# Performance work log

Hardware: AMD Instinct MI355X
Metric: run time of the kernel (lower is better)

The kernel has to match this reference:

```python
import jax, jax.numpy as jnp
import numpy as np

N_WAY = 5
K_SHOT = 5
NBNN_TOPK = 3
TEMPERATURE = 2.0
EPS = 1e-8


def setup_inputs() -> dict:
    key = jax.random.key(0)
    k1, k2, k3 = jax.random.split(key, 3)
    b, q, c, h, w = 4, 75, 640, 11, 11
    s = N_WAY * K_SHOT
    support_xf = jax.random.normal(k1, (b, s, c, h, w), jnp.float32)
    query_xf = jax.random.normal(k2, (b, q, c, h, w), jnp.float32)
    # episodes are ordered class-major: [way0 shots..., way1 shots..., ...]
    support_y = jnp.tile(jnp.repeat(jnp.arange(N_WAY, dtype=jnp.int32), K_SHOT)[None, :], (b, 1))
    query_y = jax.random.randint(k3, (b, q), 0, N_WAY, dtype=jnp.int32)
    return {"support_xf": support_xf, "query_xf": query_xf,
            "support_y": support_y, "query_y": query_y}


def _mn4_loss(support_xf, query_xf, query_y):
    b, s, c, h, w = support_xf.shape
    q = query_xf.shape[1]
    M_q = h * w
    M_s = K_SHOT * h * w

    # ---- InnerproductSimilarity (cosine) ----
    # support: [b, N, c, M_s]  (class-major grouping of shots)
    sf = support_xf.reshape(b, N_WAY, K_SHOT, c, h * w).transpose(0, 1, 3, 2, 4).reshape(b, N_WAY, c, M_s)
    qf = query_xf.reshape(b, q, c, M_q)
    sf = sf / (jnp.linalg.norm(sf, axis=2, keepdims=True) + EPS)
    qf = qf / (jnp.linalg.norm(qf, axis=2, keepdims=True) + EPS)
    # simi: [b, q, N, M_q, M_s]
    simi = jnp.einsum('bqcm,bncs->bqnms', qf, sf)

    # ---- _MNN (compensate_for_single=True branch) ----
    # merged view: [b, q, M_q, N*M_s]
    merged = simi.transpose(0, 1, 3, 2, 4).reshape(b, q, M_q, N_WAY * M_s)
    query_nearest = jnp.argmax(merged, axis=-1)          # [b, q, M_q]
    class_wise_max = simi.max(-1).max(2) + 1.0           # [b, q, M_q]
    class_m = jax.nn.one_hot(query_nearest, N_WAY * M_s, dtype=simi.dtype) * class_wise_max[..., None]
    support_nearest = jnp.argmax(class_m, axis=-2)       # [b, q, N*M_s]
    gathered = jnp.take_along_axis(support_nearest, query_nearest, axis=-1)  # [b, q, M_q]
    q_mask = (gathered == jnp.arange(M_q)[None, None, :])                    # [b, q, M_q]

    # ---- NBNN value: topk over support descriptors, masked sum over query descriptors ----
    topv = jax.lax.top_k(simi, NBNN_TOPK)[0].mean(-1)    # [b, q, N, M_q]
    query_value = (topv * q_mask[:, :, None, :].astype(topv.dtype)).sum(-1)  # [b, q, N]
    logits = query_value.reshape(b * q, N_WAY) / TEMPERATURE

    # ---- cross entropy (mean) ----
    logp = jax.nn.log_softmax(logits, axis=-1)
    y = query_y.reshape(-1)
    loss = -jnp.take_along_axis(logp, y[:, None], axis=1).mean()
    return loss


def reference(support_xf, query_xf, support_y, query_y):
    del support_y  # episodes are class-major by construction
    return _mn4_loss(support_xf, query_xf, query_y)
```

## Files before the change

kernel.cpp:

```cpp
#include <hip/hip_runtime.h>
#include <hip/hip_bf16.h>
#include <math.h>

#define BB 4
#define QQ 75
#define NBQ 300
#define CC 640
#define HW 121
#define NW 5
#define KS 5
#define SS 25
#define MS 605
#define JT 3025
#define NPAIR 38
#define PAIRS_PER_XCD 19

typedef __attribute__((ext_vector_type(8))) short short8;
typedef __attribute__((ext_vector_type(4))) float f32x4;

#define OFF_SBF   0
#define SBF_F     (BB*JT*CC/2)
#define OFF_QBF   (OFF_SBF + SBF_F)
#define QBF_F     (NBQ*HW*CC/2)
#define OFF_P     (OFF_QBF + QBF_F)
#define OFF_NRM   OFF_P

__device__ __forceinline__ void async16(const void* g, void* l) {
    __builtin_amdgcn_global_load_lds(
        (const __attribute__((address_space(1))) unsigned int*)g,
        (__attribute__((address_space(3))) unsigned int*)l, 16, 0, 0);
}

__global__ void norm_kernel(const float* __restrict__ sup, const float* __restrict__ qry,
                            float* __restrict__ nrm, float* __restrict__ out)
{
    const int blk = blockIdx.x;
    const int col = blk >> 2, r = blk & 3;
    const int hw  = threadIdx.x;
    if (blk == 0 && hw == 0) out[0] = 0.f;
    const float* src = (col < BB * SS)
        ? sup + (size_t)col * (CC * HW)
        : qry + (size_t)(col - BB * SS) * (CC * HW);
    float ss = 0.f;
    if (hw < HW) {
        const float* p = src + hw;
#pragma unroll 16
        for (int i = 0; i < CC / 4; ++i) {
            const float v = p[(size_t)(r + i * 4) * HW];
            ss = fmaf(v, v, ss);
        }
    }
    nrm[((size_t)col * 4 + r) * 128 + hw] = ss;
}

__global__ void scale_kernel(const float* __restrict__ sup, const float* __restrict__ qry,
                             const float* __restrict__ nrm,
                             __hip_bfloat16* __restrict__ Sbf, __hip_bfloat16* __restrict__ Qbf)
{
    const int blk = blockIdx.x;
    const int col = blk >> 2, qtr = blk & 3;
    const int t   = threadIdx.x;
    const float* src;
    __hip_bfloat16* dst;
    if (col < BB * SS) {
        const int b = col / SS, s = col % SS;
        const int n = s / KS, k = s % KS;
        src = sup + (size_t)col * (CC * HW);
        dst = Sbf + ((size_t)b * JT + n * MS + k * HW) * CC;
    } else {
        const int bq = col - BB * SS;
        src = qry + (size_t)bq * (CC * HW);
        dst = Qbf + (size_t)bq * (HW * CC);
    }

    __shared__ float inv[128];
    __shared__ float T[32][128];

    if (t < 128) {
        const float p0 = nrm[((size_t)col * 4 + 0) * 128 + t];
        const float p1 = nrm[((size_t)col * 4 + 1) * 128 + t];
        const float p2 = nrm[((size_t)col * 4 + 2) * 128 + t];
        const float p3 = nrm[((size_t)col * 4 + 3) * 128 + t];
        inv[t] = (t < HW) ? 1.f / (sqrtf((p0 + p2) + (p1 + p3)) + 1e-8f) : 0.f;
    }

    for (int it = 0; it < 5; ++it) {
        const int c0 = qtr * 160 + it * 32;
        __syncthreads();
#pragma unroll
        for (int i = 0; i < 16; ++i) {
            int idx = t + i * 256;
            int cc = idx >> 7, hw = idx & 127;
            if (hw < HW) T[cc][hw] = src[(size_t)(c0 + cc) * HW + hw] * inv[hw];
        }
        __syncthreads();
        const int hw = t >> 1, half = t & 1;
        if (hw < HW) {
            __hip_bfloat16 hv[16];
#pragma unroll
            for (int i = 0; i < 16; ++i) hv[i] = __float2bfloat16(T[half * 16 + i][hw]);
            int4* op = reinterpret_cast<int4*>(dst + (size_t)hw * CC + c0 + half * 16);
            op[0] = reinterpret_cast<int4*>(hv)[0];
            op[1] = reinterpret_cast<int4*>(hv)[1];
        }
    }
}

__launch_bounds__(512, 4)
__global__ void simi_kernel(const __hip_bfloat16* __restrict__ Sbf,
                            const __hip_bfloat16* __restrict__ Qbf,
                            float4* __restrict__ pout)
{
    const int xcd   = blockIdx.x & 7;
    const int local = blockIdx.x >> 3;
    const int n     = local % NW;
    const int pair  = xcd * PAIRS_PER_XCD + local / NW;
    const int b     = pair / NPAIR;
    const int pi    = pair % NPAIR;
    const bool dup  = (pi == NPAIR - 1);
    const int q0    = 2 * pi;
    const int q1    = dup ? q0 : q0 + 1;
    const int bq0   = b * QQ + q0;
    const int bq1   = b * QQ + q1;

    const int tid  = threadIdx.x;
    const int lane = tid & 63, wid = tid >> 6;
    const int l15 = lane & 15, l4 = lane >> 4;
    const int wm0 = (wid >> 1) * 64;
    const int wj0 = (wid & 1) * 64;

    const unsigned short* qb0 = (const unsigned short*)(Qbf + (size_t)bq0 * (HW * CC));
    const unsigned short* qb1 = (const unsigned short*)(Qbf + (size_t)bq1 * (HW * CC));
    const unsigned short* sbase = (const unsigned short*)(Sbf + ((size_t)b * JT + n * MS) * CC);

    __shared__ __align__(16) unsigned short AsBuf[3][256 * 32];
    __shared__ __align__(16) unsigned short BsBuf[3][128 * 32];

    const int srow = lane >> 2;
    const int kb   = (lane & 3) ^ ((lane >> 3) & 3);

    const unsigned short* aptr[2];
#pragma unroll
    for (int g = 0; g < 2; ++g) {
        int arow = wid * 32 + g * 16 + srow;
        int ml = arow & 127; ml = ml < HW ? ml : HW - 1;
        aptr[g] = ((arow >> 7) ? qb1 : qb0) + ml * CC + kb * 8;
    }
    const int jrow = wid * 16 + srow;
    const int ldsoA0 = wid * 2048 + lane * 16;
    const int ldsoA1 = ldsoA0 + 1024;
    const int ldsoB  = wid * 1024 + lane * 16;

#define STAGE(ms0_, c0_, nb_)                                                        \
    {                                                                                \
        async16(aptr[0] + (c0_), (char*)&AsBuf[nb_][0] + ldsoA0);                    \
        async16(aptr[1] + (c0_), (char*)&AsBuf[nb_][0] + ldsoA1);                    \
        int j_ = (ms0_) + jrow;                                                      \
        int jc_ = j_ < MS ? j_ : MS - 1;                                             \
        async16(sbase + jc_ * CC + kb * 8 + (c0_), (char*)&BsBuf[nb_][0] + ldsoB);   \
    }

    float rt0[4], rt1[4], rt2[4]; int ra[4];
#pragma unroll
    for (int i = 0; i < 4; ++i) { rt0[i] = -INFINITY; rt1[i] = -INFINITY; rt2[i] = -INFINITY; ra[i] = 0; }

    f32x4 acc[4][4];
#pragma unroll
    for (int ji = 0; ji < 4; ++ji)
#pragma unroll
        for (int qi = 0; qi < 4; ++qi)
#pragma unroll
            for (int r = 0; r < 4; ++r) acc[ji][qi][r] = 0.f;

    STAGE(0, 0, 0);
    int nb = 0;

    const int slot = l4 ^ ((l15 >> 1) & 3);
    const int aro  = (wm0 + l15) * 32 + slot * 8;
    const int bro  = (wj0 + l15) * 32 + slot * 8;

    for (int t = 0; t < 100; ++t) {
        const int tn = t + 1;
        const int nxt = (nb == 2) ? 0 : nb + 1;
        if (tn < 100) {
            const int nms = (tn / 20) * 128;
            const int nc  = (tn % 20) * 32;
            STAGE(nms, nc, nxt);
            asm volatile("s_waitcnt vmcnt(3)" ::: "memory");
        } else {
            asm volatile("s_waitcnt vmcnt(0)" ::: "memory");
        }
        __builtin_amdgcn_s_barrier();

        short8 af[4];
#pragma unroll
        for (int qi = 0; qi < 4; ++qi)
            af[qi] = *(const short8*)(&AsBuf[nb][0] + aro + qi * 512);

        short8 bfA = *(const short8*)(&BsBuf[nb][0] + bro);
        __builtin_amdgcn_s_setprio(1);
#pragma unroll
        for (int ji = 0; ji < 4; ++ji) {
            short8 bfB;
            if (ji < 3) bfB = *(const short8*)(&BsBuf[nb][0] + bro + (ji + 1) * 512);
#pragma unroll
            for (int qi = 0; qi < 4; ++qi)
                acc[ji][qi] = __builtin_amdgcn_mfma_f32_16x16x32_bf16(
                    bfA, af[qi], acc[ji][qi], 0, 0, 0);
            bfA = bfB;
        }
        __builtin_amdgcn_s_setprio(0);
        nb = nxt;

        if ((t % 20) == 19) {
            const int ms0 = (t / 20) * 128;
#pragma unroll
            for (int qi = 0; qi < 4; ++qi)
#pragma unroll
                for (int ji = 0; ji < 4; ++ji)
#pragma unroll
                    for (int r = 0; r < 4; ++r) {
                        const int jl = ms0 + wj0 + ji * 16 + l4 * 4 + r;
                        float v = (jl < MS) ? acc[ji][qi][r] : -INFINITY;
                        const bool gt = v > rt0[qi];
                        ra[qi] = gt ? (n * MS + jl) : ra[qi];
                        const float m1 = fminf(rt0[qi], v);
                        rt0[qi] = fmaxf(rt0[qi], v);
                        const float m2 = fminf(rt1[qi], m1);
                        rt1[qi] = fmaxf(rt1[qi], m1);
                        rt2[qi] = fmaxf(rt2[qi], m2);
                    }
#pragma unroll
            for (int ji = 0; ji < 4; ++ji)
#pragma unroll
                for (int qi = 0; qi < 4; ++qi)
#pragma unroll
                    for (int r = 0; r < 4; ++r) acc[ji][qi][r] = 0.f;
        }
    }

#pragma unroll
    for (int qi = 0; qi < 4; ++qi) {
#pragma unroll
        for (int mask = 16; mask <= 32; mask <<= 1) {
            const float o0 = __shfl_xor(rt0[qi], mask);
            const float o1 = __shfl_xor(rt1[qi], mask);
            const float o2 = __shfl_xor(rt2[qi], mask);
            const int   oa = __shfl_xor(ra[qi],  mask);
            const bool take = (o0 > rt0[qi]) || (o0 == rt0[qi] && oa < ra[qi]);
            ra[qi] = take ? oa : ra[qi];
            float m1 = fminf(rt0[qi], o0); rt0[qi] = fmaxf(rt0[qi], o0);
            float m2 = fminf(rt1[qi], m1); rt1[qi] = fmaxf(rt1[qi], m1);
            rt2[qi] = fmaxf(rt2[qi], m2);
            m1 = fminf(rt0[qi], o1); rt0[qi] = fmaxf(rt0[qi], o1);
            m2 = fminf(rt1[qi], m1); rt1[qi] = fmaxf(rt1[qi], m1);
            rt2[qi] = fmaxf(rt2[qi], m2);
            m1 = fminf(rt0[qi], o2); rt0[qi] = fmaxf(rt0[qi], o2);
            m2 = fminf(rt1[qi], m1); rt1[qi] = fmaxf(rt1[qi], m1);
            rt2[qi] = fmaxf(rt2[qi], m2);
        }
    }

    __syncthreads();
    float4* mbuf = (float4*)&AsBuf[0][0];
    if ((wid & 1) == 0 && l4 == 0) {
#pragma unroll
        for (int qi = 0; qi < 4; ++qi) {
            float4 v; v.x = rt0[qi]; v.y = rt1[qi]; v.z = rt2[qi];
            v.w = __int_as_float(ra[qi]);
            mbuf[wm0 + qi * 16 + l15] = v;
        }
    }
    __syncthreads();
    if ((wid & 1) == 1 && l4 == 0) {
#pragma unroll
        for (int qi = 0; qi < 4; ++qi) {
            const int m = wm0 + qi * 16 + l15;
            const float4 o = mbuf[m];
            const int oa = __float_as_int(o.w);
            float s0 = rt0[qi], s1 = rt1[qi], s2 = rt2[qi]; int sa = ra[qi];
            const bool take = (o.x > s0) || (o.x == s0 && oa < sa);
            sa = take ? oa : sa;
            float m1 = fminf(s0, o.x); s0 = fmaxf(s0, o.x);
            float m2 = fminf(s1, m1);  s1 = fmaxf(s1, m1);
            s2 = fmaxf(s2, m2);
            m1 = fminf(s0, o.y); s0 = fmaxf(s0, o.y);
            m2 = fminf(s1, m1);  s1 = fmaxf(s1, m1);
            s2 = fmaxf(s2, m2);
            m1 = fminf(s0, o.z); s0 = fmaxf(s0, o.z);
            m2 = fminf(s1, m1);  s1 = fmaxf(s1, m1);
            s2 = fmaxf(s2, m2);
            const int bqs = m >> 7;
            const int ml  = m & 127;
            if (ml < HW && (bqs == 0 || !dup)) {
                const int bqx = bqs ? bq1 : bq0;
                float4 v; v.x = s0; v.y = s1; v.z = s2; v.w = __int_as_float(sa);
                pout[(bqx * NW + n) * HW + ml] = v;
            }
        }
    }
#undef STAGE
}

__global__ void merge_kernel(const float4* __restrict__ pout, const int* __restrict__ qy,
                             float* __restrict__ out)
{
    const int bq  = blockIdx.x;
    const int tid = threadIdx.x;

    __shared__ float cw[128];
    __shared__ int   ag[128];
    __shared__ float tv[NW][128];
    __shared__ float maskf[128];
    __shared__ float lg[8];

    if (tid < HW) {
        float g0 = -INFINITY; int garg = 0;
#pragma unroll
        for (int n = 0; n < NW; ++n) {
            const float4 a = pout[(bq * NW + n) * HW + tid];
            if (a.x > g0) { g0 = a.x; garg = __float_as_int(a.w); }
            tv[n][tid] = (a.x + a.y + a.z) * (1.f / 3.f);
        }
        cw[tid] = g0 + 1.0f;
        ag[tid] = garg;
    }
    __syncthreads();
    if (tid < HW) {
        const float mycw = cw[tid];
        const int   myag = ag[tid];
        float ok = 1.f;
        for (int m2 = 0; m2 < HW; ++m2) {
            if (m2 == tid) continue;
            if (ag[m2] == myag) {
                float c2 = cw[m2];
                if (c2 > mycw || (c2 == mycw && m2 < tid)) ok = 0.f;
            }
        }
        maskf[tid] = ok;
    }
    __syncthreads();
    if (tid < NW) {
        float s = 0.f;
        for (int mq = 0; mq < HW; ++mq) s += maskf[mq] * tv[tid][mq];
        lg[tid] = s * 0.5f;
    }
    __syncthreads();
    if (tid == 0) {
        float m = lg[0];
#pragma unroll
        for (int n2 = 1; n2 < NW; ++n2) m = fmaxf(m, lg[n2]);
        float se = 0.f;
#pragma unroll
        for (int n2 = 0; n2 < NW; ++n2) se += expf(lg[n2] - m);
        int y = qy[bq];
        atomicAdd(out, -(lg[y] - m - logf(se)) * (1.f / NBQ));
    }
}

extern "C" void kernel_launch(void* const* d_in, const int* in_sizes, int n_in,
                              void* d_out, int out_size, void* d_ws, size_t ws_size,
                              hipStream_t stream)
{
    const float* sup = (const float*)d_in[0];
    const float* qry = (const float*)d_in[1];
    const int*   qy  = (const int*)d_in[3];
    float* out = (float*)d_out;
    float* ws  = (float*)d_ws;

    __hip_bfloat16* Sbf = (__hip_bfloat16*)(ws + OFF_SBF);
    __hip_bfloat16* Qbf = (__hip_bfloat16*)(ws + OFF_QBF);
    float4* pout = (float4*)(ws + OFF_P);
    float*  nrm  = (float*)(ws + OFF_NRM);

    hipLaunchKernelGGL(norm_kernel,  dim3((BB * SS + NBQ) * 4), dim3(128), 0, stream,
                       sup, qry, nrm, out);
    hipLaunchKernelGGL(scale_kernel, dim3((BB * SS + NBQ) * 4), dim3(256), 0, stream,
                       sup, qry, nrm, Sbf, Qbf);
    hipLaunchKernelGGL(simi_kernel, dim3(8 * PAIRS_PER_XCD * NW), dim3(512), 0, stream,
                       Sbf, Qbf, pout);
    hipLaunchKernelGGL(merge_kernel, dim3(NBQ), dim3(128), 0, stream, pout, qy, out);
}
```

Measured before the change: 393.2 us.

## Shrink simi block to 4 waves with 64-column support tiles and double buffering

The similarity kernel drops from 512 to 256 threads per block. Each wave now covers a full 64-column support tile with 64 query rows, so the cross-wave top-3 merge through LDS goes away. The K-loop runs 200 half-width steps instead of 100 and uses double buffering instead of triple, with an extra barrier each iteration. This trades a smaller LDS footprint and no final merge for twice the iterations and barriers, reloading the A tile per 64-column step, and a shallower prefetch.

```diff
diff --git a/kernel.cpp b/kernel.cpp
--- a/kernel.cpp
+++ b/kernel.cpp
@@ -106,7 +106,7 @@
     }
 }
 
-__launch_bounds__(512, 4)
+__launch_bounds__(256, 4)
 __global__ void simi_kernel(const __hip_bfloat16* __restrict__ Sbf,
                             const __hip_bfloat16* __restrict__ Qbf,
                             float4* __restrict__ pout)
@@ -126,35 +126,35 @@
     const int tid  = threadIdx.x;
     const int lane = tid & 63, wid = tid >> 6;
     const int l15 = lane & 15, l4 = lane >> 4;
-    const int wm0 = (wid >> 1) * 64;
-    const int wj0 = (wid & 1) * 64;
+    const int wm0 = wid * 64;
 
     const unsigned short* qb0 = (const unsigned short*)(Qbf + (size_t)bq0 * (HW * CC));
     const unsigned short* qb1 = (const unsigned short*)(Qbf + (size_t)bq1 * (HW * CC));
     const unsigned short* sbase = (const unsigned short*)(Sbf + ((size_t)b * JT + n * MS) * CC);
 
-    __shared__ __align__(16) unsigned short AsBuf[3][256 * 32];
-    __shared__ __align__(16) unsigned short BsBuf[3][128 * 32];
+    __shared__ __align__(16) unsigned short AsBuf[2][256 * 32];
+    __shared__ __align__(16) unsigned short BsBuf[2][64 * 32];
 
     const int srow = lane >> 2;
     const int kb   = (lane & 3) ^ ((lane >> 3) & 3);
 
-    const unsigned short* aptr[2];
-#pragma unroll
-    for (int g = 0; g < 2; ++g) {
-        int arow = wid * 32 + g * 16 + srow;
-        int ml = arow & 127; ml = ml < HW ? ml : HW - 1;
-        aptr[g] = ((arow >> 7) ? qb1 : qb0) + ml * CC + kb * 8;
+    const unsigned short* awbase = (wid < 2) ? qb0 : qb1;
+    int aoff[4];
+#pragma unroll
+    for (int g = 0; g < 4; ++g) {
+        int row = (wid & 1) * 64 + g * 16 + srow;
+        int ml = row < HW ? row : HW - 1;
+        aoff[g] = ml * CC + kb * 8;
     }
     const int jrow = wid * 16 + srow;
-    const int ldsoA0 = wid * 2048 + lane * 16;
-    const int ldsoA1 = ldsoA0 + 1024;
-    const int ldsoB  = wid * 1024 + lane * 16;
+    const int ldsoA = wid * 4096 + lane * 16;
+    const int ldsoB = wid * 1024 + lane * 16;
 
 #define STAGE(ms0_, c0_, nb_)                                                        \
     {                                                                                \
-        async16(aptr[0] + (c0_), (char*)&AsBuf[nb_][0] + ldsoA0);                    \
-        async16(aptr[1] + (c0_), (char*)&AsBuf[nb_][0] + ldsoA1);                    \
+        _Pragma("unroll")                                                            \
+        for (int g = 0; g < 4; ++g)                                                  \
+            async16(awbase + aoff[g] + (c0_), (char*)&AsBuf[nb_][0] + ldsoA + g * 1024);\
         int j_ = (ms0_) + jrow;                                                      \
         int jc_ = j_ < MS ? j_ : MS - 1;                                             \
         async16(sbase + jc_ * CC + kb * 8 + (c0_), (char*)&BsBuf[nb_][0] + ldsoB);   \
@@ -177,16 +177,15 @@
 
     const int slot = l4 ^ ((l15 >> 1) & 3);
     const int aro  = (wm0 + l15) * 32 + slot * 8;
-    const int bro  = (wj0 + l15) * 32 + slot * 8;
-
-    for (int t = 0; t < 100; ++t) {
+    const int bro  = l15 * 32 + slot * 8;
+
+    for (int t = 0; t < 200; ++t) {
         const int tn = t + 1;
-        const int nxt = (nb == 2) ? 0 : nb + 1;
-        if (tn < 100) {
-            const int nms = (tn / 20) * 128;
+        if (tn < 200) {
+            const int nms = (tn / 20) * 64;
             const int nc  = (tn % 20) * 32;
-            STAGE(nms, nc, nxt);
-            asm volatile("s_waitcnt vmcnt(3)" ::: "memory");
+            STAGE(nms, nc, nb ^ 1);
+            asm volatile("s_waitcnt vmcnt(5)" ::: "memory");
         } else {
             asm volatile("s_waitcnt vmcnt(0)" ::: "memory");
         }
@@ -210,17 +209,17 @@
             bfA = bfB;
         }
         __builtin_amdgcn_s_setprio(0);
-        nb = nxt;
+        nb ^= 1;
 
         if ((t % 20) == 19) {
-            const int ms0 = (t / 20) * 128;
+            const int ms0 = (t / 20) * 64;
 #pragma unroll
             for (int qi = 0; qi < 4; ++qi)
 #pragma unroll
                 for (int ji = 0; ji < 4; ++ji)
 #pragma unroll
                     for (int r = 0; r < 4; ++r) {
-                        const int jl = ms0 + wj0 + ji * 16 + l4 * 4 + r;
+                        const int jl = ms0 + ji * 16 + l4 * 4 + r;
                         float v = (jl < MS) ? acc[ji][qi][r] : -INFINITY;
                         const bool gt = v > rt0[qi];
                         ra[qi] = gt ? (n * MS + jl) : ra[qi];
@@ -237,6 +236,8 @@
 #pragma unroll
                     for (int r = 0; r < 4; ++r) acc[ji][qi][r] = 0.f;
         }
+
+        __builtin_amdgcn_s_barrier();
     }
 
 #pragma unroll
@@ -261,40 +262,16 @@
         }
     }
 
-    __syncthreads();
-    float4* mbuf = (float4*)&AsBuf[0][0];
-    if ((wid & 1) == 0 && l4 == 0) {
-#pragma unroll
-        for (int qi = 0; qi < 4; ++qi) {
-            float4 v; v.x = rt0[qi]; v.y = rt1[qi]; v.z = rt2[qi];
-            v.w = __int_as_float(ra[qi]);
-            mbuf[wm0 + qi * 16 + l15] = v;
-        }
-    }
-    __syncthreads();
-    if ((wid & 1) == 1 && l4 == 0) {
+    if (l4 == 0) {
 #pragma unroll
         for (int qi = 0; qi < 4; ++qi) {
             const int m = wm0 + qi * 16 + l15;
-            const float4 o = mbuf[m];
-            const int oa = __float_as_int(o.w);
-            float s0 = rt0[qi], s1 = rt1[qi], s2 = rt2[qi]; int sa = ra[qi];
-            const bool take = (o.x > s0) || (o.x == s0 && oa < sa);
-            sa = take ? oa : sa;
-            float m1 = fminf(s0, o.x); s0 = fmaxf(s0, o.x);
-            float m2 = fminf(s1, m1);  s1 = fmaxf(s1, m1);
-            s2 = fmaxf(s2, m2);
-            m1 = fminf(s0, o.y); s0 = fmaxf(s0, o.y);
-            m2 = fminf(s1, m1);  s1 = fmaxf(s1, m1);
-            s2 = fmaxf(s2, m2);
-            m1 = fminf(s0, o.z); s0 = fmaxf(s0, o.z);
-            m2 = fminf(s1, m1);  s1 = fmaxf(s1, m1);
-            s2 = fmaxf(s2, m2);
             const int bqs = m >> 7;
             const int ml  = m & 127;
             if (ml < HW && (bqs == 0 || !dup)) {
                 const int bqx = bqs ? bq1 : bq0;
-                float4 v; v.x = s0; v.y = s1; v.z = s2; v.w = __int_as_float(sa);
+                float4 v; v.x = rt0[qi]; v.y = rt1[qi]; v.z = rt2[qi];
+                v.w = __int_as_float(ra[qi]);
                 pout[(bqx * NW + n) * HW + ml] = v;
             }
         }
@@ -377,7 +354,7 @@
                        sup, qry, nrm, out);
     hipLaunchKernelGGL(scale_kernel, dim3((BB * SS + NBQ) * 4), dim3(256), 0, stream,
                        sup, qry, nrm, Sbf, Qbf);
-    hipLaunchKernelGGL(simi_kernel, dim3(8 * PAIRS_PER_XCD * NW), dim3(512), 0, stream,
+    hipLaunchKernelGGL(simi_kernel, dim3(8 * PAIRS_PER_XCD * NW), dim3(256), 0, stream,
                        Sbf, Qbf, pout);
     hipLaunchKernelGGL(merge_kernel, dim3(NBQ), dim3(128), 0, stream, pout, qy, out);
 }
```

Result: slower. 431.7 us (+9.8%).
